# Performance work log

Measured on AMD Instinct MI355X. Metric: run time of the kernel, lower is better.

The kernel has to match this reference:

```python
import jax, jax.numpy as jnp
import numpy as np

# Model constants (match init_kwargs / hardcoded values in Generator.__init__)
U, E, NH, NL = 258, 128, 2, 4
D = (U - 2) + 2 * E          # embedded_input_size = 512
B, S = 16, 192
VW, VS = 50000, 10000
DDEC, FF = 3, 4              # decoder d_model=3, dim_feedforward=4 (hardcoded)
NEG = -1e9


def layer_norm(x, g, b, eps=1e-5):
    m = jnp.mean(x, axis=-1, keepdims=True)
    v = jnp.var(x, axis=-1, keepdims=True)
    return (x - m) / jnp.sqrt(v + eps) * g + b


def mha(xq, xkv, w_qkv, b_qkv, w_o, b_o, nhead, mask=None):
    # PyTorch nn.MultiheadAttention with packed in_proj, batch_first
    d = xq.shape[-1]
    wq, wk, wv = jnp.split(w_qkv, 3, axis=0)
    bq, bk, bv = jnp.split(b_qkv, 3)
    hd = d // nhead
    Bq, Sq = xq.shape[0], xq.shape[1]
    Sk = xkv.shape[1]
    q = (xq @ wq.T + bq).reshape(Bq, Sq, nhead, hd)
    k = (xkv @ wk.T + bk).reshape(Bq, Sk, nhead, hd)
    v = (xkv @ wv.T + bv).reshape(Bq, Sk, nhead, hd)
    att = jnp.einsum('bqhd,bkhd->bhqk', q, k) / np.float32(np.sqrt(hd))
    if mask is not None:
        att = att + mask
    p = jax.nn.softmax(att, axis=-1)
    o = jnp.einsum('bhqk,bkhd->bqhd', p, v).reshape(Bq, Sq, d)
    return o @ w_o.T + b_o


def pos_enc_rows(n, d):
    # standard sinusoidal PE table (d even here); only first n rows needed
    pos = np.arange(n, dtype=np.float32)[:, None]
    div = np.exp(np.arange(0, d, 2, dtype=np.float32) * (-np.log(10000.0) / d))
    pe = np.zeros((n, d), dtype=np.float32)
    pe[:, 0::2] = np.sin(pos * div)
    pe[:, 1::2] = np.cos(pos * div)
    return jnp.asarray(pe)


def setup_inputs() -> dict:
    key = jax.random.key(0)
    ks = iter(jax.random.split(key, 64))
    def nrm(shape, s=0.05):
        return jax.random.normal(next(ks), shape, dtype=jnp.float32) * s
    feats = jax.random.normal(next(ks), (B, S, U - 2), dtype=jnp.float32)
    widx = jax.random.randint(next(ks), (B, S, 1), 0, VW).astype(jnp.float32)
    sidx = jax.random.randint(next(ks), (B, S, 1), 0, VS).astype(jnp.float32)
    src = jnp.concatenate([feats, widx, sidx], axis=2)  # (B,S,U); last 2 cols = int indices as float
    return {
        'src': src,
        'word_emb': nrm((VW, E)), 'syll_emb': nrm((VS, E)),
        'enc_qkv_w': nrm((NL, 3 * D, D)), 'enc_qkv_b': nrm((NL, 3 * D)),
        'enc_o_w': nrm((NL, D, D)), 'enc_o_b': nrm((NL, D)),
        'enc_ln1_g': jnp.ones((NL, D)), 'enc_ln1_b': jnp.zeros((NL, D)),
        'enc_ff1_w': nrm((NL, FF, D)), 'enc_ff1_b': nrm((NL, FF)),
        'enc_ff2_w': nrm((NL, D, FF)), 'enc_ff2_b': nrm((NL, D)),
        'enc_ln2_g': jnp.ones((NL, D)), 'enc_ln2_b': jnp.zeros((NL, D)),
        'normf_g': jnp.ones((D,)), 'normf_b': jnp.zeros((D,)),
        'eout_w': nrm((DDEC, D)), 'eout_b': jnp.zeros((DDEC,)),
        'dec_sa_qkv_w': nrm((NL, 3 * DDEC, DDEC)), 'dec_sa_qkv_b': nrm((NL, 3 * DDEC)),
        'dec_sa_o_w': nrm((NL, DDEC, DDEC)), 'dec_sa_o_b': nrm((NL, DDEC)),
        'dec_ca_qkv_w': nrm((NL, 3 * DDEC, DDEC)), 'dec_ca_qkv_b': nrm((NL, 3 * DDEC)),
        'dec_ca_o_w': nrm((NL, DDEC, DDEC)), 'dec_ca_o_b': nrm((NL, DDEC)),
        'dec_ln1_g': jnp.ones((NL, DDEC)), 'dec_ln1_b': jnp.zeros((NL, DDEC)),
        'dec_ln2_g': jnp.ones((NL, DDEC)), 'dec_ln2_b': jnp.zeros((NL, DDEC)),
        'dec_ln3_g': jnp.ones((NL, DDEC)), 'dec_ln3_b': jnp.zeros((NL, DDEC)),
        'dec_ff1_w': nrm((NL, FF, DDEC)), 'dec_ff1_b': nrm((NL, FF)),
        'dec_ff2_w': nrm((NL, DDEC, FF)), 'dec_ff2_b': nrm((NL, DDEC)),
    }


def reference(src, word_emb, syll_emb, enc_qkv_w, enc_qkv_b, enc_o_w, enc_o_b,
              enc_ln1_g, enc_ln1_b, enc_ff1_w, enc_ff1_b, enc_ff2_w, enc_ff2_b,
              enc_ln2_g, enc_ln2_b, normf_g, normf_b, eout_w, eout_b,
              dec_sa_qkv_w, dec_sa_qkv_b, dec_sa_o_w, dec_sa_o_b,
              dec_ca_qkv_w, dec_ca_qkv_b, dec_ca_o_w, dec_ca_o_b,
              dec_ln1_g, dec_ln1_b, dec_ln2_g, dec_ln2_b, dec_ln3_g, dec_ln3_b,
              dec_ff1_w, dec_ff1_b, dec_ff2_w, dec_ff2_b):
    # --- embed_lyrics ---
    words = jax.lax.stop_gradient(src[:, :, U - 2]).astype(jnp.int32)
    sylls = jax.lax.stop_gradient(src[:, :, U - 1]).astype(jnp.int32)
    x = jnp.concatenate([src[:, :, :U - 2], word_emb[words], syll_emb[sylls]], axis=2)  # (B,S,D)
    # --- positional encoding (faithful to original bug: x is batch-first but
    # PositionalEncoding indexes pe by dim 0 = batch, broadcasting over seq) ---
    x = x + pos_enc_rows(B, D)[:, None, :]
    # --- 4-layer post-norm TransformerEncoder (relu FFN, dropout=0) + final norm ---
    for l in range(NL):
        sa = mha(x, x, enc_qkv_w[l], enc_qkv_b[l], enc_o_w[l], enc_o_b[l], NH)
        x = layer_norm(x + sa, enc_ln1_g[l], enc_ln1_b[l])
        ff = jax.nn.relu(x @ enc_ff1_w[l].T + enc_ff1_b[l]) @ enc_ff2_w[l].T + enc_ff2_b[l]
        x = layer_norm(x + ff, enc_ln2_g[l], enc_ln2_b[l])
    x = layer_norm(x, normf_g, normf_b)
    memory = x @ eout_w.T + eout_b                      # (B,S,3)

    causal = jnp.triu(jnp.full((S, S), NEG, dtype=jnp.float32), k=1)

    def run_decoder(tgt):
        y = tgt
        for l in range(NL):
            sa = mha(y, y, dec_sa_qkv_w[l], dec_sa_qkv_b[l], dec_sa_o_w[l], dec_sa_o_b[l], 1, causal)
            y = layer_norm(y + sa, dec_ln1_g[l], dec_ln1_b[l])
            ca = mha(y, memory, dec_ca_qkv_w[l], dec_ca_qkv_b[l], dec_ca_o_w[l], dec_ca_o_b[l], 1)
            y = layer_norm(y + ca, dec_ln2_g[l], dec_ln2_b[l])
            ff = jax.nn.relu(y @ dec_ff1_w[l].T + dec_ff1_b[l]) @ dec_ff2_w[l].T + dec_ff2_b[l]
            y = layer_norm(y + ff, dec_ln3_g[l], dec_ln3_b[l])
        return y

    # prefix with a causal mask each step; running it on a fixed zero-padded
    # buffer with the same causal mask yields identical math at position i.
    def step(buf, i):
        out = run_decoder(buf)                                        # (B,S,3)
        nxt = jax.lax.dynamic_slice_in_dim(out, i, 1, axis=1)         # (B,1,3)
        buf = jax.lax.dynamic_update_slice_in_dim(buf, nxt, i + 1, axis=1)
        return buf, None

    tgt0 = jnp.zeros((B, S, DDEC), dtype=src.dtype)
    tgt, _ = jax.lax.scan(step, tgt0, jnp.arange(S - 1))
    return jnp.concatenate([tgt, src[:, :, U - 2:U - 1], src[:, :, U - 1:U]], axis=2)  # (B,S,5)
```

## Files before the change

kernel.cpp:

```cpp
#include <hip/hip_runtime.h>
#include <math.h>
#include <stdint.h>

#define BATCH 16
#define SLEN  192
#define DMODEL 512
#define UIN   258
#define NTOK  (BATCH*SLEN)
#define NLAY  4

__global__ void pe_k(float* __restrict__ pe) {
    int b = blockIdx.x;
    int i = threadIdx.x;
    float div = expf((float)(2 * i) * (-9.210340371976184f / 512.0f));
    float a = (float)b * div;
    pe[b * 512 + 2 * i]     = sinf(a);
    pe[b * 512 + 2 * i + 1] = cosf(a);
}

__global__ __launch_bounds__(256) void embed_k(
    const float* __restrict__ src, const float* __restrict__ wemb,
    const float* __restrict__ semb, const float* __restrict__ pe,
    float* __restrict__ x)
{
    int n = blockIdx.x;
    int b = n / SLEN;
    int t = threadIdx.x;
    int wi = (int)src[(size_t)n * UIN + 256];
    int si = (int)src[(size_t)n * UIN + 257];
    float v0 = src[(size_t)n * UIN + t];
    x[(size_t)n * 512 + t] = v0 + pe[b * 512 + t];
    int d = t + 256;
    float v1 = (d < 384) ? wemb[(size_t)wi * 128 + (d - 256)]
                         : semb[(size_t)si * 128 + (d - 384)];
    x[(size_t)n * 512 + d] = v1 + pe[b * 512 + d];
}

template <bool BT>
__global__ __launch_bounds__(256) void gemm64(
    const float* __restrict__ A, int lda, long long sAb, long long sAh,
    const float* __restrict__ B, int ldb, long long sBb, long long sBh,
    float* __restrict__ C, int ldc, long long sCb, long long sCh,
    int K, const float* __restrict__ bias, float alpha, int nh)
{
    int z = blockIdx.z;
    int zb = z / nh, zh = z - zb * nh;
    A += (size_t)zb * sAb + (size_t)zh * sAh;
    B += (size_t)zb * sBb + (size_t)zh * sBh;
    C += (size_t)zb * sCb + (size_t)zh * sCh;

    __shared__ float As[16][68];
    __shared__ float Bs[16][68];

    int t = threadIdx.x;
    int row0 = blockIdx.x * 64, col0 = blockIdx.y * 64;
    int lr = t >> 2, lk = (t & 3) << 2;
    int brow = t >> 4, bcol = (t & 15) << 2;
    int ty = (t >> 4) << 2, tx = (t & 15) << 2;

    float acc[4][4] = {};

    for (int k0 = 0; k0 < K; k0 += 16) {
        float4 a4 = *(const float4*)(A + (size_t)(row0 + lr) * lda + k0 + lk);
        As[lk][lr] = a4.x; As[lk + 1][lr] = a4.y; As[lk + 2][lr] = a4.z; As[lk + 3][lr] = a4.w;
        if (BT) {
            float4 b4 = *(const float4*)(B + (size_t)(col0 + lr) * ldb + k0 + lk);
            Bs[lk][lr] = b4.x; Bs[lk + 1][lr] = b4.y; Bs[lk + 2][lr] = b4.z; Bs[lk + 3][lr] = b4.w;
        } else {
            float4 b4 = *(const float4*)(B + (size_t)(k0 + brow) * ldb + col0 + bcol);
            *(float4*)&Bs[brow][bcol] = b4;
        }
        __syncthreads();
#pragma unroll
        for (int k = 0; k < 16; ++k) {
            const float4 av = *(const float4*)&As[k][ty];
            const float4 bv = *(const float4*)&Bs[k][tx];
            acc[0][0] += av.x * bv.x; acc[0][1] += av.x * bv.y; acc[0][2] += av.x * bv.z; acc[0][3] += av.x * bv.w;
            acc[1][0] += av.y * bv.x; acc[1][1] += av.y * bv.y; acc[1][2] += av.y * bv.z; acc[1][3] += av.y * bv.w;
            acc[2][0] += av.z * bv.x; acc[2][1] += av.z * bv.y; acc[2][2] += av.z * bv.z; acc[2][3] += av.z * bv.w;
            acc[3][0] += av.w * bv.x; acc[3][1] += av.w * bv.y; acc[3][2] += av.w * bv.z; acc[3][3] += av.w * bv.w;
        }
        __syncthreads();
    }
#pragma unroll
    for (int i2 = 0; i2 < 4; ++i2) {
        size_t crow = (size_t)(row0 + ty + i2) * ldc + col0 + tx;
#pragma unroll
        for (int j = 0; j < 4; ++j) {
            float v = alpha * acc[i2][j];
            if (bias) v += bias[col0 + tx + j];
            C[crow + j] = v;
        }
    }
}

__global__ __launch_bounds__(256) void enc_softmax(float* __restrict__ scores) {
    int row = blockIdx.x * 4 + (threadIdx.x >> 6);
    int lane = threadIdx.x & 63;
    float* p = scores + (size_t)row * 192;
    float v0 = p[lane], v1 = p[lane + 64], v2 = p[lane + 128];
    float m = fmaxf(fmaxf(v0, v1), v2);
#pragma unroll
    for (int s = 1; s < 64; s <<= 1) m = fmaxf(m, __shfl_xor(m, s));
    float e0 = __expf(v0 - m), e1 = __expf(v1 - m), e2 = __expf(v2 - m);
    float sm = e0 + e1 + e2;
#pragma unroll
    for (int s = 1; s < 64; s <<= 1) sm += __shfl_xor(sm, s);
    float r = 1.0f / sm;
    p[lane] = e0 * r; p[lane + 64] = e1 * r; p[lane + 128] = e2 * r;
}

__global__ __launch_bounds__(256) void res_ln(
    float* __restrict__ x, const float* __restrict__ y,
    const float* __restrict__ g, const float* __restrict__ bb)
{
    int n = blockIdx.x, t = threadIdx.x, wave = t >> 6, lane = t & 63;
    __shared__ float red[16];
    size_t base = (size_t)n * 512;
    float z0 = x[base + t] + y[base + t];
    float z1 = x[base + t + 256] + y[base + t + 256];
    float s = z0 + z1, sq = z0 * z0 + z1 * z1;
#pragma unroll
    for (int m = 1; m < 64; m <<= 1) { s += __shfl_xor(s, m); sq += __shfl_xor(sq, m); }
    if (lane == 0) { red[wave] = s; red[8 + wave] = sq; }
    __syncthreads();
    if (t == 0) {
        float S = red[0] + red[1] + red[2] + red[3];
        float Q = red[8] + red[9] + red[10] + red[11];
        float mean = S * (1.0f / 512.0f);
        float var = Q * (1.0f / 512.0f) - mean * mean;
        red[0] = mean; red[1] = 1.0f / sqrtf(var + 1e-5f);
    }
    __syncthreads();
    float mean = red[0], rs = red[1];
    x[base + t]       = (z0 - mean) * rs * g[t] + bb[t];
    x[base + t + 256] = (z1 - mean) * rs * g[t + 256] + bb[t + 256];
}

__global__ __launch_bounds__(256) void enc_ffn_ln(
    float* __restrict__ x,
    const float* __restrict__ w1, const float* __restrict__ b1,
    const float* __restrict__ w2, const float* __restrict__ b2,
    const float* __restrict__ g, const float* __restrict__ bb)
{
    int n = blockIdx.x, t = threadIdx.x, wave = t >> 6, lane = t & 63;
    __shared__ float xs[512];
    __shared__ float hs[4];
    __shared__ float red[16];
    size_t base = (size_t)n * 512;
    float x0 = x[base + t], x1 = x[base + t + 256];
    xs[t] = x0; xs[t + 256] = x1;
    __syncthreads();
    float p = 0.0f;
    for (int c = lane; c < 512; c += 64) p += xs[c] * w1[wave * 512 + c];
#pragma unroll
    for (int m = 1; m < 64; m <<= 1) p += __shfl_xor(p, m);
    if (lane == 0) hs[wave] = fmaxf(p + b1[wave], 0.0f);
    __syncthreads();
    float h0 = hs[0], h1 = hs[1], h2 = hs[2], h3 = hs[3];
    int t2 = t + 256;
    float z0 = x0 + b2[t]  + h0 * w2[t * 4]  + h1 * w2[t * 4 + 1]  + h2 * w2[t * 4 + 2]  + h3 * w2[t * 4 + 3];
    float z1 = x1 + b2[t2] + h0 * w2[t2 * 4] + h1 * w2[t2 * 4 + 1] + h2 * w2[t2 * 4 + 2] + h3 * w2[t2 * 4 + 3];
    float s = z0 + z1, sq = z0 * z0 + z1 * z1;
#pragma unroll
    for (int m = 1; m < 64; m <<= 1) { s += __shfl_xor(s, m); sq += __shfl_xor(sq, m); }
    if (lane == 0) { red[wave] = s; red[8 + wave] = sq; }
    __syncthreads();
    if (t == 0) {
        float S = red[0] + red[1] + red[2] + red[3];
        float Q = red[8] + red[9] + red[10] + red[11];
        float mean = S * (1.0f / 512.0f);
        float var = Q * (1.0f / 512.0f) - mean * mean;
        red[0] = mean; red[1] = 1.0f / sqrtf(var + 1e-5f);
    }
    __syncthreads();
    float mean = red[0], rs = red[1];
    x[base + t]  = (z0 - mean) * rs * g[t]  + bb[t];
    x[base + t2] = (z1 - mean) * rs * g[t2] + bb[t2];
}

__global__ __launch_bounds__(256) void eout_k(
    const float* __restrict__ x,
    const float* __restrict__ g, const float* __restrict__ bb,
    const float* __restrict__ ew, const float* __restrict__ eb,
    const float* __restrict__ src, float* __restrict__ mem, float* __restrict__ out)
{
    int n = blockIdx.x, t = threadIdx.x, wave = t >> 6, lane = t & 63;
    __shared__ float xs[512];
    __shared__ float red[16];
    size_t base = (size_t)n * 512;
    float z0 = x[base + t], z1 = x[base + t + 256];
    float s = z0 + z1, sq = z0 * z0 + z1 * z1;
#pragma unroll
    for (int m = 1; m < 64; m <<= 1) { s += __shfl_xor(s, m); sq += __shfl_xor(sq, m); }
    if (lane == 0) { red[wave] = s; red[8 + wave] = sq; }
    __syncthreads();
    if (t == 0) {
        float S = red[0] + red[1] + red[2] + red[3];
        float Q = red[8] + red[9] + red[10] + red[11];
        float mean = S * (1.0f / 512.0f);
        float var = Q * (1.0f / 512.0f) - mean * mean;
        red[0] = mean; red[1] = 1.0f / sqrtf(var + 1e-5f);
    }
    __syncthreads();
    float mean = red[0], rs = red[1];
    xs[t]       = (z0 - mean) * rs * g[t] + bb[t];
    xs[t + 256] = (z1 - mean) * rs * g[t + 256] + bb[t + 256];
    __syncthreads();
    if (wave < 3) {
        float p = 0.0f;
        for (int c = lane; c < 512; c += 64) p += xs[c] * ew[wave * 512 + c];
#pragma unroll
        for (int m = 1; m < 64; m <<= 1) p += __shfl_xor(p, m);
        if (lane == 0) mem[(size_t)n * 3 + wave] = p + eb[wave];
    }
    if (t == 0) {
        out[(size_t)n * 5 + 3] = src[(size_t)n * UIN + 256];
        out[(size_t)n * 5 + 4] = src[(size_t)n * UIN + 257];
    }
}

__global__ __launch_bounds__(256) void crosskv_k(
    const float* __restrict__ mem, const float* __restrict__ w, const float* __restrict__ bias,
    float* __restrict__ kmem, float* __restrict__ vmem)
{
    int idx = blockIdx.x * 256 + threadIdx.x;
    int s = idx % SLEN;
    int l = (idx / SLEN) & 3;
    int b = idx / (SLEN * 4);
    const float* m = mem + ((size_t)b * SLEN + s) * 3;
    float m0 = m[0], m1 = m[1], m2 = m[2];
    const float* wl = w + l * 27;
    const float* bl = bias + l * 9;
    float* kp = kmem + (size_t)idx * 3;
    float* vp = vmem + (size_t)idx * 3;
#pragma unroll
    for (int r = 0; r < 3; ++r) {
        kp[r] = wl[(3 + r) * 3] * m0 + wl[(3 + r) * 3 + 1] * m1 + wl[(3 + r) * 3 + 2] * m2 + bl[3 + r];
        vp[r] = wl[(6 + r) * 3] * m0 + wl[(6 + r) * 3 + 1] * m1 + wl[(6 + r) * 3 + 2] * m2 + bl[6 + r];
    }
}

template <int CTRL>
__device__ __forceinline__ float dpp_add(float x) {
    int s = __builtin_amdgcn_update_dpp(0, __float_as_int(x), CTRL, 0xf, 0xf, true);
    return x + __int_as_float(s);
}
__device__ __forceinline__ float wave_sum64(float x) {
    x = dpp_add<0x111>(x);
    x = dpp_add<0x112>(x);
    x = dpp_add<0x114>(x);
    x = dpp_add<0x118>(x);
    x = dpp_add<0x142>(x);
    x = dpp_add<0x143>(x);
    return __int_as_float(__builtin_amdgcn_readlane(__float_as_int(x), 63));
}

#define PIN(x) asm volatile("" : "+v"(x))

#define D9(n) float n##0=0.f,n##1=0.f,n##2=0.f,n##3=0.f,n##4=0.f,n##5=0.f,n##6=0.f,n##7=0.f,n##8=0.f

#define LOADM(L) do { \
    size_t base_ = (((size_t)(b * 4 + L)) * SLEN + lane) * 3; \
    Km##L##_0 = kmem[base_];       Km##L##_1 = kmem[base_ + 1];   Km##L##_2 = kmem[base_ + 2]; \
    Km##L##_3 = kmem[base_ + 192]; Km##L##_4 = kmem[base_ + 193]; Km##L##_5 = kmem[base_ + 194]; \
    Km##L##_6 = kmem[base_ + 384]; Km##L##_7 = kmem[base_ + 385]; Km##L##_8 = kmem[base_ + 386]; \
    Vm##L##_0 = vmem[base_];       Vm##L##_1 = vmem[base_ + 1];   Vm##L##_2 = vmem[base_ + 2]; \
    Vm##L##_3 = vmem[base_ + 192]; Vm##L##_4 = vmem[base_ + 193]; Vm##L##_5 = vmem[base_ + 194]; \
    Vm##L##_6 = vmem[base_ + 384]; Vm##L##_7 = vmem[base_ + 385]; Vm##L##_8 = vmem[base_ + 386]; \
} while (0)

#define PINM(L) do { \
    PIN(Km##L##_0); PIN(Km##L##_1); PIN(Km##L##_2); PIN(Km##L##_3); PIN(Km##L##_4); \
    PIN(Km##L##_5); PIN(Km##L##_6); PIN(Km##L##_7); PIN(Km##L##_8); \
    PIN(Vm##L##_0); PIN(Vm##L##_1); PIN(Vm##L##_2); PIN(Vm##L##_3); PIN(Vm##L##_4); \
    PIN(Vm##L##_5); PIN(Vm##L##_6); PIN(Vm##L##_7); PIN(Vm##L##_8); \
} while (0)

#define LN3S(Gp, Bp) { \
    const float* G_ = (Gp); const float* B_ = (Bp); \
    float mn_ = (y0 + y1 + y2) * (1.0f / 3.0f); \
    float d0_ = y0 - mn_, d1_ = y1 - mn_, d2_ = y2 - mn_; \
    float rs_ = 1.0f / sqrtf((d0_ * d0_ + d1_ * d1_ + d2_ * d2_) * (1.0f / 3.0f) + 1e-5f); \
    y0 = d0_ * rs_ * G_[0] + B_[0]; y1 = d1_ * rs_ * G_[1] + B_[1]; y2 = d2_ * rs_ * G_[2] + B_[2]; }

#define LAYER(L) { \
    const float* W  = sa_qkv_w + L * 27; const float* Bw = sa_qkv_b + L * 9; \
    float q0 = (W[0] * y0 + W[1] * y1 + W[2] * y2 + Bw[0]) * isc; \
    float q1 = (W[3] * y0 + W[4] * y1 + W[5] * y2 + Bw[1]) * isc; \
    float q2 = (W[6] * y0 + W[7] * y1 + W[8] * y2 + Bw[2]) * isc; \
    float k0 = W[9]  * y0 + W[10] * y1 + W[11] * y2 + Bw[3]; \
    float k1 = W[12] * y0 + W[13] * y1 + W[14] * y2 + Bw[4]; \
    float k2 = W[15] * y0 + W[16] * y1 + W[17] * y2 + Bw[5]; \
    float v0 = W[18] * y0 + W[19] * y1 + W[20] * y2 + Bw[6]; \
    float v1 = W[21] * y0 + W[22] * y1 + W[23] * y2 + Bw[7]; \
    float v2 = W[24] * y0 + W[25] * y1 + W[26] * y2 + Bw[8]; \
    Kc##L##_0 = m0 ? k0 : Kc##L##_0; Kc##L##_1 = m0 ? k1 : Kc##L##_1; Kc##L##_2 = m0 ? k2 : Kc##L##_2; \
    Vc##L##_0 = m0 ? v0 : Vc##L##_0; Vc##L##_1 = m0 ? v1 : Vc##L##_1; Vc##L##_2 = m0 ? v2 : Vc##L##_2; \
    Kc##L##_3 = m1 ? k0 : Kc##L##_3; Kc##L##_4 = m1 ? k1 : Kc##L##_4; Kc##L##_5 = m1 ? k2 : Kc##L##_5; \
    Vc##L##_3 = m1 ? v0 : Vc##L##_3; Vc##L##_4 = m1 ? v1 : Vc##L##_4; Vc##L##_5 = m1 ? v2 : Vc##L##_5; \
    Kc##L##_6 = m2 ? k0 : Kc##L##_6; Kc##L##_7 = m2 ? k1 : Kc##L##_7; Kc##L##_8 = m2 ? k2 : Kc##L##_8; \
    Vc##L##_6 = m2 ? v0 : Vc##L##_6; Vc##L##_7 = m2 ? v1 : Vc##L##_7; Vc##L##_8 = m2 ? v2 : Vc##L##_8; \
    float den, a0, a1, a2; \
    { \
        float sc0 = q0 * Kc##L##_0 + q1 * Kc##L##_1 + q2 * Kc##L##_2; \
        float sc1 = q0 * Kc##L##_3 + q1 * Kc##L##_4 + q2 * Kc##L##_5; \
        float sc2 = q0 * Kc##L##_6 + q1 * Kc##L##_7 + q2 * Kc##L##_8; \
        float e0 = (lane       <= i) ? __expf(sc0) : 0.0f; \
        float e1 = (lane + 64  <= i) ? __expf(sc1) : 0.0f; \
        float e2 = (lane + 128 <= i) ? __expf(sc2) : 0.0f; \
        den = e0 + e1 + e2; \
        a0 = e0 * Vc##L##_0 + e1 * Vc##L##_3 + e2 * Vc##L##_6; \
        a1 = e0 * Vc##L##_1 + e1 * Vc##L##_4 + e2 * Vc##L##_7; \
        a2 = e0 * Vc##L##_2 + e1 * Vc##L##_5 + e2 * Vc##L##_8; \
    } \
    den = wave_sum64(den); a0 = wave_sum64(a0); a1 = wave_sum64(a1); a2 = wave_sum64(a2); \
    { \
        float ri = 1.0f / den; float o0 = a0 * ri, o1 = a1 * ri, o2 = a2 * ri; \
        const float* Ow = sa_o_w + L * 9; const float* Ob = sa_o_b + L * 3; \
        y0 += Ow[0] * o0 + Ow[1] * o1 + Ow[2] * o2 + Ob[0]; \
        y1 += Ow[3] * o0 + Ow[4] * o1 + Ow[5] * o2 + Ob[1]; \
        y2 += Ow[6] * o0 + Ow[7] * o1 + Ow[8] * o2 + Ob[2]; \
    } \
    LN3S(ln1g + L * 3, ln1b + L * 3); \
    { \
        const float* Cw = ca_qkv_w + L * 27; const float* Cb = ca_qkv_b + L * 9; \
        float c0 = (Cw[0] * y0 + Cw[1] * y1 + Cw[2] * y2 + Cb[0]) * isc; \
        float c1 = (Cw[3] * y0 + Cw[4] * y1 + Cw[5] * y2 + Cb[1]) * isc; \
        float c2 = (Cw[6] * y0 + Cw[7] * y1 + Cw[8] * y2 + Cb[2]) * isc; \
        float sc0 = c0 * Km##L##_0 + c1 * Km##L##_1 + c2 * Km##L##_2; \
        float sc1 = c0 * Km##L##_3 + c1 * Km##L##_4 + c2 * Km##L##_5; \
        float sc2 = c0 * Km##L##_6 + c1 * Km##L##_7 + c2 * Km##L##_8; \
        float e0 = __expf(sc0), e1 = __expf(sc1), e2 = __expf(sc2); \
        den = e0 + e1 + e2; \
        a0 = e0 * Vm##L##_0 + e1 * Vm##L##_3 + e2 * Vm##L##_6; \
        a1 = e0 * Vm##L##_1 + e1 * Vm##L##_4 + e2 * Vm##L##_7; \
        a2 = e0 * Vm##L##_2 + e1 * Vm##L##_5 + e2 * Vm##L##_8; \
    } \
    den = wave_sum64(den); a0 = wave_sum64(a0); a1 = wave_sum64(a1); a2 = wave_sum64(a2); \
    { \
        float ri = 1.0f / den; float o0 = a0 * ri, o1 = a1 * ri, o2 = a2 * ri; \
        const float* Co = ca_o_w + L * 9; const float* Cob = ca_o_b + L * 3; \
        y0 += Co[0] * o0 + Co[1] * o1 + Co[2] * o2 + Cob[0]; \
        y1 += Co[3] * o0 + Co[4] * o1 + Co[5] * o2 + Cob[1]; \
        y2 += Co[6] * o0 + Co[7] * o1 + Co[8] * o2 + Cob[2]; \
    } \
    LN3S(ln2g + L * 3, ln2b + L * 3); \
    { \
        const float* F1 = f1w + L * 12; const float* FB1 = f1b + L * 4; \
        const float* F2 = f2w + L * 12; const float* FB2 = f2b + L * 3; \
        float h0 = fmaxf(F1[0] * y0 + F1[1]  * y1 + F1[2]  * y2 + FB1[0], 0.f); \
        float h1 = fmaxf(F1[3] * y0 + F1[4]  * y1 + F1[5]  * y2 + FB1[1], 0.f); \
        float h2 = fmaxf(F1[6] * y0 + F1[7]  * y1 + F1[8]  * y2 + FB1[2], 0.f); \
        float h3 = fmaxf(F1[9] * y0 + F1[10] * y1 + F1[11] * y2 + FB1[3], 0.f); \
        y0 += F2[0] * h0 + F2[1] * h1 + F2[2]  * h2 + F2[3]  * h3 + FB2[0]; \
        y1 += F2[4] * h0 + F2[5] * h1 + F2[6]  * h2 + F2[7]  * h3 + FB2[1]; \
        y2 += F2[8] * h0 + F2[9] * h1 + F2[10] * h2 + F2[11] * h3 + FB2[2]; \
    } \
    LN3S(ln3g + L * 3, ln3b + L * 3); \
}

__global__ __launch_bounds__(64, 1) void decoder_ar(
    const float* __restrict__ kmem, const float* __restrict__ vmem,
    const float* __restrict__ sa_qkv_w, const float* __restrict__ sa_qkv_b,
    const float* __restrict__ sa_o_w, const float* __restrict__ sa_o_b,
    const float* __restrict__ ca_qkv_w, const float* __restrict__ ca_qkv_b,
    const float* __restrict__ ca_o_w, const float* __restrict__ ca_o_b,
    const float* __restrict__ ln1g, const float* __restrict__ ln1b,
    const float* __restrict__ ln2g, const float* __restrict__ ln2b,
    const float* __restrict__ ln3g, const float* __restrict__ ln3b,
    const float* __restrict__ f1w, const float* __restrict__ f1b,
    const float* __restrict__ f2w, const float* __restrict__ f2b,
    float* __restrict__ out)
{
    int b = blockIdx.x, lane = threadIdx.x;
    const float isc = 0.57735026918962576f;

    D9(Km0_); D9(Km1_); D9(Km2_); D9(Km3_);
    D9(Vm0_); D9(Vm1_); D9(Vm2_); D9(Vm3_);
    D9(Kc0_); D9(Kc1_); D9(Kc2_); D9(Kc3_);
    D9(Vc0_); D9(Vc1_); D9(Vc2_); D9(Vc3_);

    LOADM(0); LOADM(1); LOADM(2); LOADM(3);
    PINM(0); PINM(1); PINM(2); PINM(3);

    if (lane < 3) out[(size_t)(b * SLEN) * 5 + lane] = 0.0f;

    float y0 = 0.0f, y1 = 0.0f, y2 = 0.0f;

    for (int i = 0; i < SLEN - 1; ++i) {
        bool m0 = (i == lane);
        bool m1 = (i == lane + 64);
        bool m2 = (i == lane + 128);
        LAYER(0)
        LAYER(1)
        LAYER(2)
        LAYER(3)
        if (lane == 0) {
            size_t o = (size_t)(b * SLEN + i + 1) * 5;
            out[o] = y0; out[o + 1] = y1; out[o + 2] = y2;
        }
    }
}

extern "C" void kernel_launch(void* const* d_in, const int* in_sizes, int n_in,
                              void* d_out, int out_size, void* d_ws, size_t ws_size,
                              hipStream_t stream)
{
    const float* src   = (const float*)d_in[0];
    const float* wemb  = (const float*)d_in[1];
    const float* semb  = (const float*)d_in[2];
    const float* eqkvw = (const float*)d_in[3];
    const float* eqkvb = (const float*)d_in[4];
    const float* eow   = (const float*)d_in[5];
    const float* eob   = (const float*)d_in[6];
    const float* eln1g = (const float*)d_in[7];
    const float* eln1b = (const float*)d_in[8];
    const float* ef1w  = (const float*)d_in[9];
    const float* ef1b  = (const float*)d_in[10];
    const float* ef2w  = (const float*)d_in[11];
    const float* ef2b  = (const float*)d_in[12];
    const float* eln2g = (const float*)d_in[13];
    const float* eln2b = (const float*)d_in[14];
    const float* nfg   = (const float*)d_in[15];
    const float* nfb   = (const float*)d_in[16];
    const float* eoutw = (const float*)d_in[17];
    const float* eoutb = (const float*)d_in[18];
    const float* dsaqw = (const float*)d_in[19];
    const float* dsaqb = (const float*)d_in[20];
    const float* dsaow = (const float*)d_in[21];
    const float* dsaob = (const float*)d_in[22];
    const float* dcaqw = (const float*)d_in[23];
    const float* dcaqb = (const float*)d_in[24];
    const float* dcaow = (const float*)d_in[25];
    const float* dcaob = (const float*)d_in[26];
    const float* dln1g = (const float*)d_in[27];
    const float* dln1b = (const float*)d_in[28];
    const float* dln2g = (const float*)d_in[29];
    const float* dln2b = (const float*)d_in[30];
    const float* dln3g = (const float*)d_in[31];
    const float* dln3b = (const float*)d_in[32];
    const float* df1w  = (const float*)d_in[33];
    const float* df1b  = (const float*)d_in[34];
    const float* df2w  = (const float*)d_in[35];
    const float* df2b  = (const float*)d_in[36];
    float* out = (float*)d_out;

    float* ws = (float*)d_ws;
    float* pe     = ws;
    float* x      = pe + 8192;
    float* qkv    = x + 1572864;
    float* scores = qkv + 4718592;
    float* attn   = scores + 1179648;
    float* mem    = attn + 1572864;
    float* kmem   = mem + 9216;
    float* vmem   = kmem + 36864;
    float* yb     = qkv;

    pe_k<<<16, 256, 0, stream>>>(pe);
    embed_k<<<NTOK, 256, 0, stream>>>(src, wemb, semb, pe, x);

    for (int l = 0; l < NLAY; ++l) {
        gemm64<true><<<dim3(48, 24, 1), 256, 0, stream>>>(
            x, 512, 0, 0,
            eqkvw + (size_t)l * 786432, 512, 0, 0,
            qkv, 1536, 0, 0,
            512, eqkvb + l * 1536, 1.0f, 1);
        gemm64<true><<<dim3(3, 3, 32), 256, 0, stream>>>(
            qkv, 1536, 294912, 256,
            qkv + 512, 1536, 294912, 256,
            scores, 192, 73728, 36864,
            256, nullptr, 0.0625f, 2);
        enc_softmax<<<1536, 256, 0, stream>>>(scores);
        gemm64<false><<<dim3(3, 4, 32), 256, 0, stream>>>(
            scores, 192, 73728, 36864,
            qkv + 1024, 1536, 294912, 256,
            attn, 512, 98304, 256,
            192, nullptr, 1.0f, 2);
        gemm64<true><<<dim3(48, 8, 1), 256, 0, stream>>>(
            attn, 512, 0, 0,
            eow + (size_t)l * 262144, 512, 0, 0,
            yb, 512, 0, 0,
            512, eob + l * 512, 1.0f, 1);
        res_ln<<<NTOK, 256, 0, stream>>>(x, yb, eln1g + l * 512, eln1b + l * 512);
        enc_ffn_ln<<<NTOK, 256, 0, stream>>>(x, ef1w + l * 2048, ef1b + l * 4,
                                             ef2w + l * 2048, ef2b + l * 512,
                                             eln2g + l * 512, eln2b + l * 512);
    }

    eout_k<<<NTOK, 256, 0, stream>>>(x, nfg, nfb, eoutw, eoutb, src, mem, out);
    crosskv_k<<<48, 256, 0, stream>>>(mem, dcaqw, dcaqb, kmem, vmem);
    decoder_ar<<<BATCH, 64, 0, stream>>>(kmem, vmem,
        dsaqw, dsaqb, dsaow, dsaob, dcaqw, dcaqb, dcaow, dcaob,
        dln1g, dln1b, dln2g, dln2b, dln3g, dln3b,
        df1w, df1b, df2w, df2b, out);
}
```

Baseline: 1.765 ms.

## Add 128x128 QKV GEMM, split decoder loop by causal segment, use fast rcp/rsq

Replaces the encoder QKV projection GEMM with a new 128x128-tile kernel that gives each thread an 8x8 register micro-tile, for more reuse per shared-memory load. Splits the autoregressive decoder loop into three phases by how many 64-key segments are active, so masked segments no longer run score and exp work and the cache-update selects shrink. Also swaps 1/sqrt and division for the hardware rsq and rcp intrinsics. This risks register pressure in the larger GEMM and slightly lower numeric precision.

```diff
diff --git a/kernel.cpp b/kernel.cpp
--- a/kernel.cpp
+++ b/kernel.cpp
@@ -94,6 +94,60 @@
     }
 }
 
+__global__ __launch_bounds__(256) void gemm128_bt(
+    const float* __restrict__ A, int lda,
+    const float* __restrict__ B, int ldb,
+    float* __restrict__ C, int ldc,
+    int K, const float* __restrict__ bias)
+{
+    __shared__ float As[16][132];
+    __shared__ float Bs[16][132];
+    int t = threadIdx.x;
+    int row0 = blockIdx.x * 128, col0 = blockIdx.y * 128;
+    int lr = t >> 2;
+    int lk = (t & 3) << 2;
+    int ty = (t >> 4) << 2;
+    int tx = (t & 15) << 2;
+
+    float acc[8][8] = {};
+
+    for (int k0 = 0; k0 < K; k0 += 16) {
+        float4 a0 = *(const float4*)(A + (size_t)(row0 + lr) * lda + k0 + lk);
+        float4 a1 = *(const float4*)(A + (size_t)(row0 + 64 + lr) * lda + k0 + lk);
+        float4 b0 = *(const float4*)(B + (size_t)(col0 + lr) * ldb + k0 + lk);
+        float4 b1 = *(const float4*)(B + (size_t)(col0 + 64 + lr) * ldb + k0 + lk);
+        As[lk][lr] = a0.x; As[lk + 1][lr] = a0.y; As[lk + 2][lr] = a0.z; As[lk + 3][lr] = a0.w;
+        As[lk][64 + lr] = a1.x; As[lk + 1][64 + lr] = a1.y; As[lk + 2][64 + lr] = a1.z; As[lk + 3][64 + lr] = a1.w;
+        Bs[lk][lr] = b0.x; Bs[lk + 1][lr] = b0.y; Bs[lk + 2][lr] = b0.z; Bs[lk + 3][lr] = b0.w;
+        Bs[lk][64 + lr] = b1.x; Bs[lk + 1][64 + lr] = b1.y; Bs[lk + 2][64 + lr] = b1.z; Bs[lk + 3][64 + lr] = b1.w;
+        __syncthreads();
+#pragma unroll
+        for (int k = 0; k < 16; ++k) {
+            float4 av0 = *(const float4*)&As[k][ty];
+            float4 av1 = *(const float4*)&As[k][64 + ty];
+            float4 bv0 = *(const float4*)&Bs[k][tx];
+            float4 bv1 = *(const float4*)&Bs[k][64 + tx];
+            float a_[8] = {av0.x, av0.y, av0.z, av0.w, av1.x, av1.y, av1.z, av1.w};
+            float b_[8] = {bv0.x, bv0.y, bv0.z, bv0.w, bv1.x, bv1.y, bv1.z, bv1.w};
+#pragma unroll
+            for (int ii = 0; ii < 8; ++ii)
+#pragma unroll
+                for (int jj = 0; jj < 8; ++jj)
+                    acc[ii][jj] += a_[ii] * b_[jj];
+        }
+        __syncthreads();
+    }
+#pragma unroll
+    for (int ii = 0; ii < 8; ++ii) {
+        int row = row0 + ((ii < 4) ? (ty + ii) : (64 + ty + ii - 4));
+#pragma unroll
+        for (int jj = 0; jj < 8; ++jj) {
+            int col = col0 + ((jj < 4) ? (tx + jj) : (64 + tx + jj - 4));
+            C[(size_t)row * ldc + col] = acc[ii][jj] + bias[col];
+        }
+    }
+}
+
 __global__ __launch_bounds__(256) void enc_softmax(float* __restrict__ scores) {
     int row = blockIdx.x * 4 + (threadIdx.x >> 6);
     int lane = threadIdx.x & 63;
@@ -281,10 +335,10 @@
     const float* G_ = (Gp); const float* B_ = (Bp); \
     float mn_ = (y0 + y1 + y2) * (1.0f / 3.0f); \
     float d0_ = y0 - mn_, d1_ = y1 - mn_, d2_ = y2 - mn_; \
-    float rs_ = 1.0f / sqrtf((d0_ * d0_ + d1_ * d1_ + d2_ * d2_) * (1.0f / 3.0f) + 1e-5f); \
+    float rs_ = __builtin_amdgcn_rsqf((d0_ * d0_ + d1_ * d1_ + d2_ * d2_) * (1.0f / 3.0f) + 1e-5f); \
     y0 = d0_ * rs_ * G_[0] + B_[0]; y1 = d1_ * rs_ * G_[1] + B_[1]; y2 = d2_ * rs_ * G_[2] + B_[2]; }
 
-#define LAYER(L) { \
+#define LAYER(L, NS) { \
     const float* W  = sa_qkv_w + L * 27; const float* Bw = sa_qkv_b + L * 9; \
     float q0 = (W[0] * y0 + W[1] * y1 + W[2] * y2 + Bw[0]) * isc; \
     float q1 = (W[3] * y0 + W[4] * y1 + W[5] * y2 + Bw[1]) * isc; \
@@ -295,28 +349,36 @@
     float v0 = W[18] * y0 + W[19] * y1 + W[20] * y2 + Bw[6]; \
     float v1 = W[21] * y0 + W[22] * y1 + W[23] * y2 + Bw[7]; \
     float v2 = W[24] * y0 + W[25] * y1 + W[26] * y2 + Bw[8]; \
-    Kc##L##_0 = m0 ? k0 : Kc##L##_0; Kc##L##_1 = m0 ? k1 : Kc##L##_1; Kc##L##_2 = m0 ? k2 : Kc##L##_2; \
-    Vc##L##_0 = m0 ? v0 : Vc##L##_0; Vc##L##_1 = m0 ? v1 : Vc##L##_1; Vc##L##_2 = m0 ? v2 : Vc##L##_2; \
-    Kc##L##_3 = m1 ? k0 : Kc##L##_3; Kc##L##_4 = m1 ? k1 : Kc##L##_4; Kc##L##_5 = m1 ? k2 : Kc##L##_5; \
-    Vc##L##_3 = m1 ? v0 : Vc##L##_3; Vc##L##_4 = m1 ? v1 : Vc##L##_4; Vc##L##_5 = m1 ? v2 : Vc##L##_5; \
-    Kc##L##_6 = m2 ? k0 : Kc##L##_6; Kc##L##_7 = m2 ? k1 : Kc##L##_7; Kc##L##_8 = m2 ? k2 : Kc##L##_8; \
-    Vc##L##_6 = m2 ? v0 : Vc##L##_6; Vc##L##_7 = m2 ? v1 : Vc##L##_7; Vc##L##_8 = m2 ? v2 : Vc##L##_8; \
+    { bool ms = (i == lane + 64 * ((NS) - 1)); \
+      if ((NS) == 1) { \
+        Kc##L##_0 = ms ? k0 : Kc##L##_0; Kc##L##_1 = ms ? k1 : Kc##L##_1; Kc##L##_2 = ms ? k2 : Kc##L##_2; \
+        Vc##L##_0 = ms ? v0 : Vc##L##_0; Vc##L##_1 = ms ? v1 : Vc##L##_1; Vc##L##_2 = ms ? v2 : Vc##L##_2; \
+      } else if ((NS) == 2) { \
+        Kc##L##_3 = ms ? k0 : Kc##L##_3; Kc##L##_4 = ms ? k1 : Kc##L##_4; Kc##L##_5 = ms ? k2 : Kc##L##_5; \
+        Vc##L##_3 = ms ? v0 : Vc##L##_3; Vc##L##_4 = ms ? v1 : Vc##L##_4; Vc##L##_5 = ms ? v2 : Vc##L##_5; \
+      } else { \
+        Kc##L##_6 = ms ? k0 : Kc##L##_6; Kc##L##_7 = ms ? k1 : Kc##L##_7; Kc##L##_8 = ms ? k2 : Kc##L##_8; \
+        Vc##L##_6 = ms ? v0 : Vc##L##_6; Vc##L##_7 = ms ? v1 : Vc##L##_7; Vc##L##_8 = ms ? v2 : Vc##L##_8; \
+      } } \
     float den, a0, a1, a2; \
     { \
         float sc0 = q0 * Kc##L##_0 + q1 * Kc##L##_1 + q2 * Kc##L##_2; \
-        float sc1 = q0 * Kc##L##_3 + q1 * Kc##L##_4 + q2 * Kc##L##_5; \
-        float sc2 = q0 * Kc##L##_6 + q1 * Kc##L##_7 + q2 * Kc##L##_8; \
-        float e0 = (lane       <= i) ? __expf(sc0) : 0.0f; \
-        float e1 = (lane + 64  <= i) ? __expf(sc1) : 0.0f; \
-        float e2 = (lane + 128 <= i) ? __expf(sc2) : 0.0f; \
-        den = e0 + e1 + e2; \
-        a0 = e0 * Vc##L##_0 + e1 * Vc##L##_3 + e2 * Vc##L##_6; \
-        a1 = e0 * Vc##L##_1 + e1 * Vc##L##_4 + e2 * Vc##L##_7; \
-        a2 = e0 * Vc##L##_2 + e1 * Vc##L##_5 + e2 * Vc##L##_8; \
+        float e0 = ((NS) == 1) ? ((lane <= i) ? __expf(sc0) : 0.0f) : __expf(sc0); \
+        den = e0; a0 = e0 * Vc##L##_0; a1 = e0 * Vc##L##_1; a2 = e0 * Vc##L##_2; \
+        if ((NS) >= 2) { \
+            float sc1 = q0 * Kc##L##_3 + q1 * Kc##L##_4 + q2 * Kc##L##_5; \
+            float e1 = ((NS) == 2) ? ((lane + 64 <= i) ? __expf(sc1) : 0.0f) : __expf(sc1); \
+            den += e1; a0 += e1 * Vc##L##_3; a1 += e1 * Vc##L##_4; a2 += e1 * Vc##L##_5; \
+        } \
+        if ((NS) >= 3) { \
+            float sc2 = q0 * Kc##L##_6 + q1 * Kc##L##_7 + q2 * Kc##L##_8; \
+            float e2 = (lane + 128 <= i) ? __expf(sc2) : 0.0f; \
+            den += e2; a0 += e2 * Vc##L##_6; a1 += e2 * Vc##L##_7; a2 += e2 * Vc##L##_8; \
+        } \
     } \
     den = wave_sum64(den); a0 = wave_sum64(a0); a1 = wave_sum64(a1); a2 = wave_sum64(a2); \
     { \
-        float ri = 1.0f / den; float o0 = a0 * ri, o1 = a1 * ri, o2 = a2 * ri; \
+        float ri = __builtin_amdgcn_rcpf(den); float o0 = a0 * ri, o1 = a1 * ri, o2 = a2 * ri; \
         const float* Ow = sa_o_w + L * 9; const float* Ob = sa_o_b + L * 3; \
         y0 += Ow[0] * o0 + Ow[1] * o1 + Ow[2] * o2 + Ob[0]; \
         y1 += Ow[3] * o0 + Ow[4] * o1 + Ow[5] * o2 + Ob[1]; \
@@ -339,7 +401,7 @@
     } \
     den = wave_sum64(den); a0 = wave_sum64(a0); a1 = wave_sum64(a1); a2 = wave_sum64(a2); \
     { \
-        float ri = 1.0f / den; float o0 = a0 * ri, o1 = a1 * ri, o2 = a2 * ri; \
+        float ri = __builtin_amdgcn_rcpf(den); float o0 = a0 * ri, o1 = a1 * ri, o2 = a2 * ri; \
         const float* Co = ca_o_w + L * 9; const float* Cob = ca_o_b + L * 3; \
         y0 += Co[0] * o0 + Co[1] * o1 + Co[2] * o2 + Cob[0]; \
         y1 += Co[3] * o0 + Co[4] * o1 + Co[5] * o2 + Cob[1]; \
@@ -360,6 +422,12 @@
     LN3S(ln3g + L * 3, ln3b + L * 3); \
 }
 
+#define STEP_OUT { \
+    if (lane == 0) { \
+        size_t o = (size_t)(b * SLEN + i + 1) * 5; \
+        out[o] = y0; out[o + 1] = y1; out[o + 2] = y2; \
+    } }
+
 __global__ __launch_bounds__(64, 1) void decoder_ar(
     const float* __restrict__ kmem, const float* __restrict__ vmem,
     const float* __restrict__ sa_qkv_w, const float* __restrict__ sa_qkv_b,
@@ -388,19 +456,10 @@
 
     float y0 = 0.0f, y1 = 0.0f, y2 = 0.0f;
 
-    for (int i = 0; i < SLEN - 1; ++i) {
-        bool m0 = (i == lane);
-        bool m1 = (i == lane + 64);
-        bool m2 = (i == lane + 128);
-        LAYER(0)
-        LAYER(1)
-        LAYER(2)
-        LAYER(3)
-        if (lane == 0) {
-            size_t o = (size_t)(b * SLEN + i + 1) * 5;
-            out[o] = y0; out[o + 1] = y1; out[o + 2] = y2;
-        }
-    }
+    int i = 0;
+    for (; i < 64; ++i)  { LAYER(0, 1) LAYER(1, 1) LAYER(2, 1) LAYER(3, 1) STEP_OUT }
+    for (; i < 128; ++i) { LAYER(0, 2) LAYER(1, 2) LAYER(2, 2) LAYER(3, 2) STEP_OUT }
+    for (; i < SLEN - 1; ++i) { LAYER(0, 3) LAYER(1, 3) LAYER(2, 3) LAYER(3, 3) STEP_OUT }
 }
 
 extern "C" void kernel_launch(void* const* d_in, const int* in_sizes, int n_in,
@@ -461,11 +520,11 @@
     embed_k<<<NTOK, 256, 0, stream>>>(src, wemb, semb, pe, x);
 
     for (int l = 0; l < NLAY; ++l) {
-        gemm64<true><<<dim3(48, 24, 1), 256, 0, stream>>>(
-            x, 512, 0, 0,
-            eqkvw + (size_t)l * 786432, 512, 0, 0,
-            qkv, 1536, 0, 0,
-            512, eqkvb + l * 1536, 1.0f, 1);
+        gemm128_bt<<<dim3(24, 12), 256, 0, stream>>>(
+            x, 512,
+            eqkvw + (size_t)l * 786432, 512,
+            qkv, 1536,
+            512, eqkvb + l * 1536);
         gemm64<true><<<dim3(3, 3, 32), 256, 0, stream>>>(
             qkv, 1536, 294912, 256,
             qkv + 512, 1536, 294912, 256,
```

Result: no change. 1.791 ms (+1.5%).
